# Kernel tuning notes

Measured on AMD Instinct MI355X. Metric: run time of the kernel, lower is better.

## Reference

```python
import jax, jax.numpy as jnp
import numpy as np

DIM = 16      # memory_columns = dim
HEADS = 2
ROWS = 2 * HEADS * DIM          # memory_rows = 64
COLS = DIM                      # 16
PREC = 16                       # memory_precision
MC = ROWS * COLS * PREC         # memory_cell_amount = 16384
EMB = 64                        # embedding_size
RH = 2                          # read_heads
OUT = ROWS * COLS               # output_size = memory_size = 1024
UNITS = OUT + 2 * ROWS + 2 * COLS  # controller LSTM units = 1184
DSTEPS = 2                      # discretization_steps

# standard sinusoidal positional encoding over ROWS+1 positions
_L = ROWS + 1
_pos = np.arange(_L, dtype=np.float32)[:, None]
_i = np.arange(EMB)[None, :]
_ang = _pos / np.power(10000.0, (2 * (_i // 2)) / EMB)
PE = jnp.asarray(np.where(_i % 2 == 0, np.sin(_ang), np.cos(_ang)).astype(np.float32))[None]  # (1, 65, 64)

# non-trainable (default) conductance ODE constants, stacked per synapse type:
# [input, recurrent, inhibitory, leakage]
COND = jnp.array([0.07915332, 1.0334609, 1.3365093, 0.4505964], jnp.float32)
MEAN = jnp.array([0.5, 0.07879465, 0.06618887, 0.0], jnp.float32)
STD = jnp.array([100.0, 100.0, 100.0, 1.0], jnp.float32)
TGT = jnp.array([1.5931877, 1.4378392, 0.0, 0.0], jnp.float32)
PART_STEP = jnp.float32(1.5573331 / DSTEPS)  # step_size / discretization_steps (capacitance = 1)


def _forward(queries, values, Wi, bi, Wm, bm, Wq, bq, Wk, bk, Wv, bv, Wo, bo, Wx, bl):
    B, Q, _ = queries.shape
    V = values.shape[1]
    dq = jnp.repeat(queries[:, :, None, :], V, 2)          # (B,Q,V,dim)
    dv = jnp.repeat(values[:, None, :, :], Q, 1)           # (B,Q,V,dim)
    mli = jnp.concatenate([dq, dv], -1).reshape(B * Q, V, 2 * DIM)  # (128,V,32)
    xs = jnp.swapaxes(mli, 0, 1)                           # (V,128,32) time-major
    BQ = B * Q                                             # == 128 (hardcoded in source)
    pot0 = jnp.broadcast_to(jnp.array([0.0, 1.0], jnp.float32), (BQ, MC, 2))
    scale = 1.0 / jnp.sqrt(jnp.float32(EMB))               # MHA key_dim = EMB

    def step(pot, x_t):
        # read memory row contents (even-indexed state entries = potentials)
        mem = pot[..., 0].reshape(BQ, ROWS, COLS * PREC)   # (128,64,256)
        emb_mem = mem @ Wm + bm                            # (128,64,64)
        emb_in = (x_t @ Wi + bi)[:, None, :]               # (128,1,64)
        aug = jnp.concatenate([emb_in, emb_mem], 1) + PE   # (128,65,64)
        # multi-head self-attention; only the row-0 query is kept downstream
        q = jnp.einsum('bd,dhk->bhk', aug[:, 0], Wq) + bq
        k = jnp.einsum('bld,dhk->blhk', aug, Wk) + bk
        v = jnp.einsum('bld,dhk->blhk', aug, Wv) + bv
        attn = jax.nn.softmax(jnp.einsum('bhk,blhk->bhl', q, k) * scale, -1)
        ctx = jnp.einsum('bhl,blhk->bhk', attn, v)
        o = jnp.einsum('bhk,hkd->bd', ctx, Wo) + bo        # (128,64)
        # LSTM controller over a length-1 sequence with zero initial state:
        # recurrent term h0 @ Wr vanishes, so z = x @ Wx + b
        z = o @ Wx + bl                                    # (128,4*1184)
        zi, zf, zg, zo = jnp.split(z, 4, -1)
        c = jax.nn.sigmoid(zi) * jnp.tanh(zg)
        h = jax.nn.sigmoid(zo) * jnp.tanh(c)
        out = h[:, :OUT]                                   # (128,1024)
        # multi-step Euler integration of the conductance ODE
        inp = jnp.zeros_like(pot)                          # neuron_inputs = zeros
        p = pot
        for _ in range(DSTEPS):
            pre = jnp.stack([inp, p, p[..., ::-1], jnp.full_like(p, jnp.inf)], -1)  # (128,MC,2,4)
            sig = jax.nn.sigmoid(STD * (pre - MEAN))
            curr = COND * sig * (TGT - p[..., None])
            p = p + jnp.sum(curr, -1) * PART_STEP
        return p, out

    _, ys = jax.lax.scan(step, pot0, xs)
    # keras RNN default: last-step output; then reshape as in MemoryLayerAttention.call
    return ys[-1].reshape(-1, Q, DIM)                      # (512,16,16)


def setup_inputs():
    key = jax.random.key(0)
    ks = jax.random.split(key, 10)
    n = lambda k, s: jax.random.normal(k, s, jnp.float32) * 0.05
    return {
        'queries': jax.random.normal(ks[0], (8, 16, DIM), jnp.float32),
        'values': jax.random.normal(ks[1], (8, 8, DIM), jnp.float32),
        'Wi': n(ks[2], (2 * DIM, EMB)), 'bi': jnp.zeros((EMB,), jnp.float32),
        'Wm': n(ks[3], (COLS * PREC, EMB)), 'bm': jnp.zeros((EMB,), jnp.float32),
        'Wq': n(ks[4], (EMB, RH, EMB)), 'bq': jnp.zeros((RH, EMB), jnp.float32),
        'Wk': n(ks[5], (EMB, RH, EMB)), 'bk': jnp.zeros((RH, EMB), jnp.float32),
        'Wv': n(ks[6], (EMB, RH, EMB)), 'bv': jnp.zeros((RH, EMB), jnp.float32),
        'Wo': n(ks[7], (RH, EMB, EMB)), 'bo': jnp.zeros((EMB,), jnp.float32),
        'Wx': n(ks[8], (EMB, 4 * UNITS)), 'bl': jnp.zeros((4 * UNITS,), jnp.float32),
    }


def reference(queries, values, Wi, bi, Wm, bm, Wq, bq, Wk, bk, Wv, bv, Wo, bo, Wx, bl):
    return _forward(queries, values, Wi, bi, Wm, bm, Wq, bq, Wk, bk, Wv, bv, Wo, bo, Wx, bl)
```

## Files before the change

### kernel.cpp

```cpp
#include <hip/hip_runtime.h>
#include <math.h>

#define EMB 64
#define ROWS 64
#define UNITS 1184
#define OUTN 1024
#define ZCOLS 4736

__device__ float g_kv[16384];

__device__ __forceinline__ float stable_sigmoid(float x) {
    if (x >= 0.0f) return 1.0f / (1.0f + expf(-x));
    float e = expf(x);
    return e / (1.0f + e);
}

__device__ __forceinline__ float pot_sub(float pc, float po) {
    float t0 = 0.07915332f * stable_sigmoid(100.0f * (0.0f - 0.5f))        * (1.5931877f - pc);
    float t1 = 1.0334609f  * stable_sigmoid(100.0f * (pc - 0.07879465f))   * (1.4378392f - pc);
    float t2 = 1.3365093f  * stable_sigmoid(100.0f * (po - 0.06618887f))   * (0.0f - pc);
    float t3 = 0.4505964f  * 1.0f                                          * (0.0f - pc);
    return pc + (t0 + t1 + t2 + t3) * (1.5573331f / 2.0f);
}

__device__ __forceinline__ float pot_a7() {
    float p0 = 0.0f, p1 = 1.0f;
    for (int t = 0; t < 7; ++t)
        for (int s = 0; s < 2; ++s) {
            float n0 = pot_sub(p0, p1);
            float n1 = pot_sub(p1, p0);
            p0 = n0; p1 = n1;
        }
    return p0;
}

__global__ __launch_bounds__(256)
void precompute_kv(const float* __restrict__ Wm, const float* __restrict__ bm,
                   const float* __restrict__ Wk, const float* __restrict__ bk,
                   const float* __restrict__ Wv, const float* __restrict__ bv) {
    __shared__ float part[4][EMB];
    __shared__ float s_m[EMB];
    __shared__ float aug[ROWS][EMB];
    const int tid = threadIdx.x;

    {
        const int rg = tid >> 6, c = tid & 63;
        float s = 0.0f;
        #pragma unroll 8
        for (int r = 0; r < 64; ++r) s += Wm[(rg * 64 + r) * EMB + c];
        part[rg][c] = s;
    }
    __syncthreads();
    if (tid < EMB) {
        const float a = pot_a7();
        s_m[tid] = a * (part[0][tid] + part[1][tid] + part[2][tid] + part[3][tid]) + bm[tid];
    }
    __syncthreads();

    for (int idx = tid; idx < ROWS * EMB; idx += 256) {
        const int l = idx >> 6, d = idx & 63;
        const float inv = exp2f(-(float)(2 * (d >> 1)) * (13.287712379549449f / 64.0f));
        const float ang = (float)(l + 1) * inv;
        const float pe  = (d & 1) ? cosf(ang) : sinf(ang);
        aug[l][d] = s_m[d] + pe;
    }
    __syncthreads();

    const int idx = blockIdx.x * 256 + tid;
    const int isv = idx >> 13;
    const int r   = idx & 8191;
    const int l   = r >> 7;
    const int t   = r & 127;
    const float* W  = isv ? Wv : Wk;
    const float* bb = isv ? bv : bk;
    float s = bb[t];
    #pragma unroll 16
    for (int d = 0; d < EMB; ++d) s += aug[l][d] * W[d * 128 + t];
    g_kv[idx] = s;
}

__global__ __launch_bounds__(256)
void attend_out(const float* __restrict__ queries, const float* __restrict__ values,
                const float* __restrict__ Wi, const float* __restrict__ bi,
                const float* __restrict__ Wq, const float* __restrict__ bq,
                const float* __restrict__ Wk, const float* __restrict__ bk,
                const float* __restrict__ Wv, const float* __restrict__ bv,
                const float* __restrict__ Wo, const float* __restrict__ bo,
                const float* __restrict__ Wx, const float* __restrict__ bl,
                float* __restrict__ out) {
    const int b = blockIdx.x >> 2, tid = threadIdx.x;
    __shared__ float x[32], e[EMB], qv[128], k0[128], v0[128], att[2][65], ctx[128], o[EMB];

    if (tid < 16)      x[tid] = queries[b * 16 + tid];
    else if (tid < 32) x[tid] = values[(b >> 4) * 128 + 112 + (tid - 16)];
    __syncthreads();

    if (tid < EMB) {
        float s = bi[tid] + ((tid & 1) ? 1.0f : 0.0f);
        #pragma unroll 8
        for (int i = 0; i < 32; ++i) s += x[i] * Wi[i * EMB + tid];
        e[tid] = s;
    }
    __syncthreads();

    if (tid < 128) {
        float s = bq[tid];
        #pragma unroll 8
        for (int d = 0; d < EMB; ++d) s += e[d] * Wq[d * 128 + tid];
        qv[tid] = s;
        float sv = bv[tid];
        #pragma unroll 8
        for (int d = 0; d < EMB; ++d) sv += e[d] * Wv[d * 128 + tid];
        v0[tid] = sv;
    } else {
        const int t = tid - 128;
        float s = bk[t];
        #pragma unroll 8
        for (int d = 0; d < EMB; ++d) s += e[d] * Wk[d * 128 + t];
        k0[t] = s;
    }
    __syncthreads();

    if (tid < 130) {
        const int h = tid & 1, l = tid >> 1;
        const float* qh = &qv[h * 64];
        float s = 0.0f;
        if (l == 0) {
            #pragma unroll 8
            for (int d = 0; d < 64; ++d) s += qh[d] * k0[h * 64 + d];
        } else {
            const float* kr = &g_kv[(l - 1) * 128 + h * 64];
            #pragma unroll 8
            for (int d = 0; d < 64; ++d) s += qh[d] * kr[d];
        }
        att[h][l] = s * 0.125f;
    }
    __syncthreads();

    if (tid < 2) {
        float m = -1e30f;
        for (int l = 0; l < 65; ++l) m = fmaxf(m, att[tid][l]);
        float sum = 0.0f;
        for (int l = 0; l < 65; ++l) { float ex = expf(att[tid][l] - m); att[tid][l] = ex; sum += ex; }
        float inv = 1.0f / sum;
        for (int l = 0; l < 65; ++l) att[tid][l] *= inv;
    }
    __syncthreads();

    if (tid < 128) {
        const int h = tid >> 6;
        float s = att[h][0] * v0[tid];
        const float* vm = &g_kv[8192 + tid];
        #pragma unroll 8
        for (int l = 0; l < 64; ++l) s += att[h][l + 1] * vm[l * 128];
        ctx[tid] = s;
    }
    __syncthreads();

    if (tid < 64) {
        float s = bo[tid];
        #pragma unroll 16
        for (int t = 0; t < 128; ++t) s += ctx[t] * Wo[t * 64 + tid];
        o[tid] = s;
    }
    __syncthreads();

    const int j = ((blockIdx.x & 3) << 8) | tid;
    float zi = bl[j], zg = bl[2 * UNITS + j], zo = bl[3 * UNITS + j];
    const float* col = Wx + j;
    #pragma unroll 16
    for (int d = 0; d < EMB; ++d) {
        const float od = o[d];
        const float* row = col + d * ZCOLS;
        zi += od * row[0];
        zg += od * row[2 * UNITS];
        zo += od * row[3 * UNITS];
    }
    const float c = stable_sigmoid(zi) * tanhf(zg);
    out[b * OUTN + j] = stable_sigmoid(zo) * tanhf(c);
}

extern "C" void kernel_launch(void* const* d_in, const int* in_sizes, int n_in,
                              void* d_out, int out_size, void* d_ws, size_t ws_size,
                              hipStream_t stream) {
    const float* queries = (const float*)d_in[0];
    const float* values  = (const float*)d_in[1];
    const float* Wi = (const float*)d_in[2];
    const float* bi = (const float*)d_in[3];
    const float* Wm = (const float*)d_in[4];
    const float* bm = (const float*)d_in[5];
    const float* Wq = (const float*)d_in[6];
    const float* bq = (const float*)d_in[7];
    const float* Wk = (const float*)d_in[8];
    const float* bk = (const float*)d_in[9];
    const float* Wv = (const float*)d_in[10];
    const float* bv = (const float*)d_in[11];
    const float* Wo = (const float*)d_in[12];
    const float* bo = (const float*)d_in[13];
    const float* Wx = (const float*)d_in[14];
    const float* bl = (const float*)d_in[15];
    float* out = (float*)d_out;
    (void)d_ws; (void)ws_size;

    precompute_kv<<<64, 256, 0, stream>>>(Wm, bm, Wk, bk, Wv, bv);
    attend_out<<<512, 256, 0, stream>>>(queries, values, Wi, bi, Wq, bq, Wk, bk,
                                        Wv, bv, Wo, bo, Wx, bl, out);
}
```

Before: 119.6 us.

## Prefetch weights into cache early and parallelize softmax with wavefront shuffles

Both kernels issue dummy loads of weight lines (Wk/Wv, Wx, Wq/Wk/Wv/Wo, Wi) at kernel start so later dependent reads hit in cache. Each load result is kept alive with an empty asm statement so the compiler does not drop it. The two-thread serial softmax is replaced by a wavefront-wide shuffle reduction, with the 65th score handled separately by lane 63. Other changes: a branchless stable sigmoid, computing pot_a7 in every thread before the barrier, and reading queries/values directly instead of staging them in shared memory. The prefetch adds extra memory traffic and register pressure in the first blocks.

```diff
diff --git a/kernel.cpp b/kernel.cpp
--- a/kernel.cpp
+++ b/kernel.cpp
@@ -10,9 +10,9 @@
 __device__ float g_kv[16384];
 
 __device__ __forceinline__ float stable_sigmoid(float x) {
-    if (x >= 0.0f) return 1.0f / (1.0f + expf(-x));
-    float e = expf(x);
-    return e / (1.0f + e);
+    const float e = expf(-fabsf(x));
+    const float r = 1.0f / (1.0f + e);
+    return (x >= 0.0f) ? r : 1.0f - r;
 }
 
 __device__ __forceinline__ float pot_sub(float pc, float po) {
@@ -43,16 +43,20 @@
     __shared__ float aug[ROWS][EMB];
     const int tid = threadIdx.x;
 
+    float pf;
     {
-        const int rg = tid >> 6, c = tid & 63;
-        float s = 0.0f;
-        #pragma unroll 8
-        for (int r = 0; r < 64; ++r) s += Wm[(rg * 64 + r) * EMB + c];
-        part[rg][c] = s;
-    }
+        const int o1 = tid * 16;
+        pf = Wk[o1] + Wk[o1 + 4096] + Wv[o1] + Wv[o1 + 4096];
+    }
+
+    float s = 0.0f;
+    const int rg = tid >> 6, c = tid & 63;
+    #pragma unroll 8
+    for (int r = 0; r < 64; ++r) s += Wm[(rg * 64 + r) * EMB + c];
+    const float a = pot_a7();
+    part[rg][c] = s;
     __syncthreads();
     if (tid < EMB) {
-        const float a = pot_a7();
         s_m[tid] = a * (part[0][tid] + part[1][tid] + part[2][tid] + part[3][tid]) + bm[tid];
     }
     __syncthreads();
@@ -73,10 +77,11 @@
     const int t   = r & 127;
     const float* W  = isv ? Wv : Wk;
     const float* bb = isv ? bv : bk;
-    float s = bb[t];
+    float sv = bb[t];
     #pragma unroll 16
-    for (int d = 0; d < EMB; ++d) s += aug[l][d] * W[d * 128 + t];
-    g_kv[idx] = s;
+    for (int d = 0; d < EMB; ++d) sv += aug[l][d] * W[d * 128 + t];
+    asm volatile("" :: "v"(pf));
+    g_kv[idx] = sv;
 }
 
 __global__ __launch_bounds__(256)
@@ -89,16 +94,34 @@
                 const float* __restrict__ Wx, const float* __restrict__ bl,
                 float* __restrict__ out) {
     const int b = blockIdx.x >> 2, tid = threadIdx.x;
-    __shared__ float x[32], e[EMB], qv[128], k0[128], v0[128], att[2][65], ctx[128], o[EMB];
-
-    if (tid < 16)      x[tid] = queries[b * 16 + tid];
-    else if (tid < 32) x[tid] = values[(b >> 4) * 128 + 112 + (tid - 16)];
-    __syncthreads();
+    __shared__ float e[EMB], qv[128], k0[128], v0[128], att[2][66], ctx[128], o[EMB];
+
+    float pf = 0.0f;
+    if (blockIdx.x < 4) {
+        const int j0 = (blockIdx.x & 3) << 8;
+        #pragma unroll
+        for (int kk = 0; kk < 12; ++kk) {
+            const int li = tid * 12 + kk;
+            const int z  = li >> 10;
+            const int r  = (li >> 4) & 63;
+            const int cc = (li & 15) << 4;
+            const int zoff = (z == 0) ? 0 : ((z == 1) ? 2 * UNITS : 3 * UNITS);
+            pf += Wx[r * ZCOLS + zoff + j0 + cc];
+        }
+        const float* pw = (blockIdx.x == 0) ? Wq : (blockIdx.x == 1) ? Wk
+                        : (blockIdx.x == 2) ? Wv : Wo;
+        pf += pw[tid * 16] + pw[tid * 16 + 4096];
+        if (blockIdx.x == 0 && tid < 128) pf += Wi[tid * 16];
+    }
 
     if (tid < EMB) {
         float s = bi[tid] + ((tid & 1) ? 1.0f : 0.0f);
-        #pragma unroll 8
-        for (int i = 0; i < 32; ++i) s += x[i] * Wi[i * EMB + tid];
+        const float* qp = queries + b * 16;
+        const float* vp = values + (b >> 4) * 128 + 112;
+        #pragma unroll
+        for (int i = 0; i < 16; ++i) s += qp[i] * Wi[i * EMB + tid];
+        #pragma unroll
+        for (int i = 0; i < 16; ++i) s += vp[i] * Wi[(16 + i) * EMB + tid];
         e[tid] = s;
     }
     __syncthreads();
@@ -121,29 +144,41 @@
     }
     __syncthreads();
 
-    if (tid < 130) {
-        const int h = tid & 1, l = tid >> 1;
+    if (tid < 128) {
+        const int h = tid >> 6, p = tid & 63;
         const float* qh = &qv[h * 64];
         float s = 0.0f;
-        if (l == 0) {
+        if (p == 0) {
             #pragma unroll 8
             for (int d = 0; d < 64; ++d) s += qh[d] * k0[h * 64 + d];
         } else {
-            const float* kr = &g_kv[(l - 1) * 128 + h * 64];
+            const float* kr = &g_kv[(p - 1) * 128 + h * 64];
             #pragma unroll 8
             for (int d = 0; d < 64; ++d) s += qh[d] * kr[d];
         }
-        att[h][l] = s * 0.125f;
-    }
-    __syncthreads();
-
-    if (tid < 2) {
-        float m = -1e30f;
-        for (int l = 0; l < 65; ++l) m = fmaxf(m, att[tid][l]);
-        float sum = 0.0f;
-        for (int l = 0; l < 65; ++l) { float ex = expf(att[tid][l] - m); att[tid][l] = ex; sum += ex; }
-        float inv = 1.0f / sum;
-        for (int l = 0; l < 65; ++l) att[tid][l] *= inv;
+        s *= 0.125f;
+        float s64 = -1e30f;
+        if (p == 63) {
+            const float* kr = &g_kv[63 * 128 + h * 64];
+            float t64 = 0.0f;
+            #pragma unroll 8
+            for (int d = 0; d < 64; ++d) t64 += qh[d] * kr[d];
+            s64 = t64 * 0.125f;
+        }
+        s64 = __shfl(s64, 63, 64);
+        float m = s;
+        #pragma unroll
+        for (int mask = 1; mask < 64; mask <<= 1) m = fmaxf(m, __shfl_xor(m, mask, 64));
+        m = fmaxf(m, s64);
+        const float ex  = expf(s - m);
+        const float e64 = expf(s64 - m);
+        float sum = ex;
+        #pragma unroll
+        for (int mask = 1; mask < 64; mask <<= 1) sum += __shfl_xor(sum, mask, 64);
+        sum += e64;
+        const float inv = 1.0f / sum;
+        att[h][p] = ex * inv;
+        if (p == 63) att[h][64] = e64 * inv;
     }
     __syncthreads();
 
@@ -164,6 +199,8 @@
         o[tid] = s;
     }
     __syncthreads();
+
+    asm volatile("" :: "v"(pf));
 
     const int j = ((blockIdx.x & 3) << 8) | tid;
     float zi = bl[j], zg = bl[2 * UNITS + j], zo = bl[3 * UNITS + j];
```

Result: faster. 115.1 us (-3.7%).
